# Kernel optimization log

Measured on AMD Instinct MI355X. Metric: run time of the kernel, lower is better.

Reference implementation:

```python
import jax, jax.numpy as jnp
import numpy as np

HEAD_NUM = 16
PAD = 0.0
MASKS_FUTURE = True


def setup_inputs() -> dict:
    key = jax.random.key(0)
    ks = jax.random.split(key, 7)
    B, S, D = 2, 2048, 1024
    scale = 0.02
    return {
        "q": jax.random.normal(ks[0], (B, S, D), dtype=jnp.float32),
        "k": jax.random.normal(ks[1], (B, S, D), dtype=jnp.float32),
        "v": jax.random.normal(ks[2], (B, S, D), dtype=jnp.float32),
        "w_q": jax.random.normal(ks[3], (D, D), dtype=jnp.float32) * scale,
        "w_k": jax.random.normal(ks[4], (D, D), dtype=jnp.float32) * scale,
        "w_v": jax.random.normal(ks[5], (D, D), dtype=jnp.float32) * scale,
        "w_o": jax.random.normal(ks[6], (D, D), dtype=jnp.float32) * scale,
    }


def _split_head(x):
    # [B, S, D] -> [B, H, S, D/H]
    B, S, D = x.shape
    return x.reshape(B, S, HEAD_NUM, D // HEAD_NUM).transpose(0, 2, 1, 3)


def reference(q, k, v, w_q, w_k, w_v, w_o):
    qp = _split_head(q @ w_q)  # [B, H, Sq, dk]
    kp = _split_head(k @ w_k)  # [B, H, Sk, dk]
    vp = _split_head(v @ w_v)  # [B, H, Sk, dv]
    d_k = qp.shape[-1]
    scores = jnp.einsum("bhqd,bhkd->bhqk", qp, kp) / jnp.sqrt(jnp.float32(d_k))
    # mask where scores equal PAD (faithful to tf.equal(head_qk, PAD))
    mask = scores == PAD
    if MASKS_FUTURE:
        # tf.linalg.band_part(mask, -1, 0): keep lower triangle, zero elsewhere
        Sq, Sk = scores.shape[-2], scores.shape[-1]
        tril = jnp.tril(jnp.ones((Sq, Sk), dtype=bool))
        mask = mask & tril
    neg = jnp.finfo(jnp.float32).min
    scores = jnp.where(mask, neg, scores)
    attn = jax.nn.softmax(scores, axis=-1)
    # keep_prob = 1.0 -> dropout is identity
    attn = jnp.where(mask, PAD, attn)
    out = jnp.einsum("bhqk,bhkd->bhqd", attn, vp)  # [B, H, Sq, dv/H]
    B, H, S, dh = out.shape
    concat = out.transpose(0, 2, 1, 3).reshape(B, S, H * dh)
    return concat @ w_o
```

## Files before the change

### kernel.cpp

```cpp
#include <hip/hip_runtime.h>
#include <hip/hip_bf16.h>

typedef unsigned short u16;
typedef unsigned int u32;
typedef short short8 __attribute__((ext_vector_type(8)));
typedef float float4v __attribute__((ext_vector_type(4)));
typedef u32 u32x2 __attribute__((ext_vector_type(2)));

#define SEQ 2048
#define DIM 1024
#define NHEAD 16
#define MROWS 4096
#define NE ((size_t)MROWS * DIM)
#define WN ((size_t)DIM * DIM)

#if __has_builtin(__builtin_amdgcn_exp2f)
#define EXP2(x) __builtin_amdgcn_exp2f(x)
#else
#define EXP2(x) exp2f(x)
#endif

__device__ inline u16 f2bf(float f) {
    union { float f; unsigned u; } v; v.f = f;
    unsigned r = v.u + 0x7fffu + ((v.u >> 16) & 1u);
    return (u16)(r >> 16);
}
__device__ inline float bf2f(u16 s) {
    union { unsigned u; float f; } v; v.u = ((unsigned)s) << 16;
    return v.f;
}
__device__ inline u32 pk2bf(float a, float b) {
    union { __hip_bfloat162 h; u32 u; } cv;
    cv.h = __float22bfloat162_rn(float2{a, b});
    return cv.u;
}
__device__ inline void gld16(const void* g, void* l) {
    __builtin_amdgcn_global_load_lds(
        (const __attribute__((address_space(1))) void*)g,
        (__attribute__((address_space(3))) void*)l, 16, 0, 0);
}

__global__ __launch_bounds__(256) void prep(
    const float* __restrict__ q, const float* __restrict__ k,
    const float* __restrict__ v, const float* __restrict__ w_q,
    const float* __restrict__ w_k, const float* __restrict__ w_v,
    const float* __restrict__ w_o, u16* __restrict__ Abf, u16* __restrict__ Wt)
{
    __shared__ u16 T[64 * 66];
    const int bx = blockIdx.x;
    const int tid = threadIdx.x;

    if (bx < 6144) {
        const int z = bx >> 11, xb = bx & 2047;
        const float* s = (z == 0) ? q : (z == 1) ? k : v;
        const size_t i = ((size_t)xb * 256 + tid) * 8;
        float4v a = *(const float4v*)(s + i);
        float4v b = *(const float4v*)(s + i + 4);
        short8 o;
        for (int e = 0; e < 4; e++) { o[e] = (short)f2bf(a[e]); o[4 + e] = (short)f2bf(b[e]); }
        *(short8*)(Abf + (size_t)z * NE + i) = o;
        return;
    }

    const int t = bx - 6144;
    const int z = t & 3, tile = t >> 2;
    const float* src = (z == 0) ? w_o : (z == 1) ? w_q : (z == 2) ? w_k : w_v;
    const int kt = (tile >> 4) * 64, nt = (tile & 15) * 64;
    {
        const int row = tid >> 2, cg = (tid & 3) * 16;
        const float* sp = src + (size_t)(kt + row) * DIM + nt + cg;
        for (int i4 = 0; i4 < 4; i4++) {
            float4v f = *(const float4v*)(sp + i4 * 4);
            for (int e = 0; e < 4; e++)
                T[row * 66 + cg + i4 * 4 + e] = f2bf(f[e]);
        }
    }
    __syncthreads();
    {
        const int nr = tid >> 2, kg = (tid & 3) * 16;
        u16* dp = Wt + (size_t)z * WN + (size_t)(nt + nr) * DIM + kt + kg;
        short8 o0, o1;
        for (int e = 0; e < 8; e++) {
            o0[e] = (short)T[(kg + e) * 66 + nr];
            o1[e] = (short)T[(kg + 8 + e) * 66 + nr];
        }
        *(short8*)(dp) = o0;
        *(short8*)(dp + 8) = o1;
    }
}

__global__ __launch_bounds__(256) void gemm_qkv(
    const u16* __restrict__ Abf, const u16* __restrict__ Wtg, u16* __restrict__ QKVb)
{
    __shared__ u16 SMEM[2 * 128 * 64];
    u16* Alds = SMEM;
    u16* Wlds = SMEM + 128 * 64;

    const int z = blockIdx.z;
    const u16* A = Abf + (size_t)z * NE;
    const u16* W = Wtg + (size_t)(z + 1) * WN;

    const int tid = threadIdx.x;
    const int lane = tid & 63, w = tid >> 6;
    const int quad = lane >> 4, l16 = lane & 15;
    const int wr = w >> 1, wc = w & 1;
    const int m0 = blockIdx.x * 128, n0 = blockIdx.y * 128;

    float4v acc[4][4];
    float4v vz = {0.f, 0.f, 0.f, 0.f};
    for (int i = 0; i < 4; i++)
        for (int j = 0; j < 4; j++) acc[i][j] = vz;

    for (int k0 = 0; k0 < DIM; k0 += 64) {
        for (int i = 0; i < 4; i++) {
            const int c = tid + i * 256;
            const int row = c >> 3, scc = (c & 7) ^ (row & 7);
            gld16(A + (size_t)(m0 + row) * DIM + k0 + scc * 8, &Alds[c * 8]);
            gld16(W + (size_t)(n0 + row) * DIM + k0 + scc * 8, &Wlds[c * 8]);
        }
        __syncthreads();

        for (int s = 0; s < 2; s++) {
            short8 a[4], b[4];
            for (int i = 0; i < 4; i++) {
                const int row = wr * 64 + i * 16 + l16;
                a[i] = *(const short8*)&Alds[row * 64 + (((s * 4 + quad) ^ (row & 7)) * 8)];
            }
            for (int j = 0; j < 4; j++) {
                const int row = wc * 64 + j * 16 + l16;
                b[j] = *(const short8*)&Wlds[row * 64 + (((s * 4 + quad) ^ (row & 7)) * 8)];
            }
            for (int i = 0; i < 4; i++)
                for (int j = 0; j < 4; j++)
                    acc[i][j] = __builtin_amdgcn_mfma_f32_16x16x32_bf16(a[i], b[j], acc[i][j], 0, 0, 0);
        }
        __syncthreads();
    }

    if (z < 2) {
        const float sc = (z == 0) ? 0.125f * 1.44269504088896f : 1.0f;
        for (int i = 0; i < 4; i++) {
            int row = m0 + wr * 64 + i * 16 + quad * 4;
            for (int j = 0; j < 4; j++) {
                int col = n0 + wc * 64 + j * 16 + l16;
                for (int r = 0; r < 4; r++)
                    QKVb[(size_t)z * NE + (size_t)(row + r) * DIM + col] = f2bf(acc[i][j][r] * sc);
            }
        }
        return;
    }

    u16* T = SMEM;
    for (int i = 0; i < 4; i++)
        for (int j = 0; j < 4; j++) {
            const int d = wc * 64 + j * 16 + l16;
            for (int r = 0; r < 4; r++) {
                const int s = wr * 64 + i * 16 + quad * 4 + r;
                T[d * 128 + (((s >> 3) ^ (d & 7)) * 8) + (s & 7)] = f2bf(acc[i][j][r]);
            }
        }
    __syncthreads();
    {
        u16* Vt = QKVb + 2 * NE;
        const int b = m0 >> 11, s_loc = m0 & 2047, h0 = n0 >> 6;
        const int c = lane & 15;
        for (int p = 0; p < 8; p++) {
            const int d = w * 32 + (lane >> 4) * 8 + p;
            short8 val = *(const short8*)&T[d * 128 + ((c ^ (d & 7)) * 8)];
            u16* dp = Vt + ((size_t)(b * 16 + h0 + (d >> 6)) * 64 + (d & 63)) * SEQ + s_loc + c * 8;
            *(short8*)dp = val;
        }
    }
}

__global__ __launch_bounds__(256) void gemm_out(
    const u16* __restrict__ Cb, const u16* __restrict__ Wtg, float* __restrict__ out)
{
    __shared__ u16 Alds[64 * 64];
    __shared__ u16 Wlds[128 * 64];
    const u16* W = Wtg;

    const int tid = threadIdx.x;
    const int lane = tid & 63, w = tid >> 6;
    const int quad = lane >> 4, l16 = lane & 15;
    const int wr = w >> 1, wc = w & 1;
    const int m0 = blockIdx.x * 64, n0 = blockIdx.y * 128;

    float4v acc[2][4];
    float4v vz = {0.f, 0.f, 0.f, 0.f};
    for (int i = 0; i < 2; i++)
        for (int j = 0; j < 4; j++) acc[i][j] = vz;

    for (int k0 = 0; k0 < DIM; k0 += 64) {
        for (int i = 0; i < 2; i++) {
            const int c = tid + i * 256;
            const int row = c >> 3, scc = (c & 7) ^ (row & 7);
            gld16(Cb + (size_t)(m0 + row) * DIM + k0 + scc * 8, &Alds[c * 8]);
        }
        for (int i = 0; i < 4; i++) {
            const int c = tid + i * 256;
            const int row = c >> 3, scc = (c & 7) ^ (row & 7);
            gld16(W + (size_t)(n0 + row) * DIM + k0 + scc * 8, &Wlds[c * 8]);
        }
        __syncthreads();

        for (int s = 0; s < 2; s++) {
            short8 a[2], b[4];
            for (int i = 0; i < 2; i++) {
                const int row = wr * 32 + i * 16 + l16;
                a[i] = *(const short8*)&Alds[row * 64 + (((s * 4 + quad) ^ (row & 7)) * 8)];
            }
            for (int j = 0; j < 4; j++) {
                const int row = wc * 64 + j * 16 + l16;
                b[j] = *(const short8*)&Wlds[row * 64 + (((s * 4 + quad) ^ (row & 7)) * 8)];
            }
            for (int i = 0; i < 2; i++)
                for (int j = 0; j < 4; j++)
                    acc[i][j] = __builtin_amdgcn_mfma_f32_16x16x32_bf16(a[i], b[j], acc[i][j], 0, 0, 0);
        }
        __syncthreads();
    }

    for (int i = 0; i < 2; i++) {
        int row = m0 + wr * 32 + i * 16 + quad * 4;
        for (int j = 0; j < 4; j++) {
            int col = n0 + wc * 64 + j * 16 + l16;
            for (int r = 0; r < 4; r++)
                out[(size_t)(row + r) * DIM + col] = acc[i][j][r];
        }
    }
}

__global__ __launch_bounds__(256, 4) void attn_kernel(
    const u16* __restrict__ Q, const u16* __restrict__ K,
    const u16* __restrict__ Vtg, u16* __restrict__ O)
{
    __shared__ u16 Klds[128 * 64];
    __shared__ u16 Vt[64 * 128];
    __shared__ float Llds[4][32];
    float* bufA = (float*)Klds;
    float* bufB = (float*)Vt;

    const int bh = blockIdx.x;
    const int q0 = blockIdx.y * 32;
    const int tid = threadIdx.x;
    const int lane = tid & 63, w = tid >> 6;
    const int quad = lane >> 4, l16 = lane & 15;

    const size_t base = (size_t)(bh >> 4) * SEQ * DIM + (bh & 15) * 64;
    const u16* Qp = Q + base;
    const u16* Kp = K + base;
    u16* Op = O + base;
    const u16* Vp = Vtg + (size_t)bh * 64 * SEQ;

    short8 qb[2][2];
    for (int qc = 0; qc < 2; qc++)
        for (int s = 0; s < 2; s++)
            qb[qc][s] = *(const short8*)(Qp + (size_t)(q0 + qc * 16 + l16) * DIM + s * 32 + quad * 8);

    float4v acc[2][4];
    float4v vz = {0.f, 0.f, 0.f, 0.f};
    for (int qc = 0; qc < 2; qc++)
        for (int nb = 0; nb < 4; nb++) acc[qc][nb] = vz;
    float lp[2] = {0.f, 0.f};

    u16* pw = Klds + w * 32 * 64;

    for (int kt = 0; kt < SEQ / 128; kt++) {
        const int k0 = kt * 128;
        for (int i = 0; i < 4; i++) {
            const int ck = tid + i * 256;
            const int rk = ck >> 3, sk = (ck & 7) ^ (rk & 7);
            gld16(Kp + (size_t)(k0 + rk) * DIM + sk * 8, &Klds[ck * 8]);
            const int cv = tid + i * 256;
            const int dv = cv >> 4, pv = cv & 15;
            const int sv = (pv & 8) | ((pv ^ (dv & 7)) & 7);
            gld16(Vp + (size_t)dv * SEQ + k0 + sv * 8, &Vt[cv * 8]);
        }
        __syncthreads();

        short8 ka[2][2];
        for (int kr = 0; kr < 2; kr++) {
            const int row = w * 32 + kr * 16 + l16;
            ka[kr][0] = *(const short8*)&Klds[row * 64 + ((quad ^ (l16 & 7)) * 8)];
            ka[kr][1] = *(const short8*)&Klds[row * 64 + (((4 + quad) ^ (l16 & 7)) * 8)];
        }

        float4v st[2][2];
        for (int kr = 0; kr < 2; kr++)
            for (int qc = 0; qc < 2; qc++) {
                float4v t = __builtin_amdgcn_mfma_f32_16x16x32_bf16(ka[kr][0], qb[qc][0], vz, 0, 0, 0);
                st[kr][qc] = __builtin_amdgcn_mfma_f32_16x16x32_bf16(ka[kr][1], qb[qc][1], t, 0, 0, 0);
            }

        for (int kr = 0; kr < 2; kr++)
            for (int qc = 0; qc < 2; qc++) {
                float p0 = EXP2(st[kr][qc][0]), p1 = EXP2(st[kr][qc][1]);
                float p2 = EXP2(st[kr][qc][2]), p3 = EXP2(st[kr][qc][3]);
                lp[qc] += (p0 + p1) + (p2 + p3);
                u32x2 pk; pk[0] = pk2bf(p0, p1); pk[1] = pk2bf(p2, p3);
                *(u32x2*)((u32*)pw + (qc * 16 + l16) * 20 + kr * 8 + quad * 2) = pk;
            }
        asm volatile("" ::: "memory");

        short8 pa[2], vb[4];
        for (int qc = 0; qc < 2; qc++)
            pa[qc] = *(const short8*)&pw[(qc * 16 + l16) * 40 + quad * 8];
        for (int nb = 0; nb < 4; nb++) {
            const int gk = w * 4 + quad;
            const int pos = (gk & 8) | ((gk ^ (l16 & 7)) & 7);
            vb[nb] = *(const short8*)&Vt[(nb * 16 + l16) * 128 + pos * 8];
        }
        for (int qc = 0; qc < 2; qc++)
            for (int nb = 0; nb < 4; nb++)
                acc[qc][nb] = __builtin_amdgcn_mfma_f32_16x16x32_bf16(pa[qc], vb[nb], acc[qc][nb], 0, 0, 0);
        __syncthreads();
    }

    for (int qc = 0; qc < 2; qc++) {
        lp[qc] += __shfl_xor(lp[qc], 16);
        lp[qc] += __shfl_xor(lp[qc], 32);
    }
    if (quad == 0)
        for (int qc = 0; qc < 2; qc++) Llds[w][qc * 16 + l16] = lp[qc];

    if (w == 0 || w == 2) {
        float* buf = (w == 0) ? bufA : bufB;
        for (int qc = 0; qc < 2; qc++)
            for (int nb = 0; nb < 4; nb++)
                for (int r = 0; r < 4; r++)
                    buf[(qc * 16 + quad * 4 + r) * 64 + nb * 16 + l16] = acc[qc][nb][r];
    }
    __syncthreads();
    if (w == 1 || w == 3) {
        float* buf = (w == 1) ? bufA : bufB;
        for (int qc = 0; qc < 2; qc++)
            for (int nb = 0; nb < 4; nb++)
                for (int r = 0; r < 4; r++)
                    buf[(qc * 16 + quad * 4 + r) * 64 + nb * 16 + l16] += acc[qc][nb][r];
    }
    __syncthreads();

    {
        const int q = tid >> 3, dg = (tid & 7) * 8;
        const float l = Llds[0][q] + Llds[1][q] + Llds[2][q] + Llds[3][q];
        const float inv = 1.0f / l;
        short8 o;
        for (int e = 0; e < 8; e++)
            o[e] = (short)f2bf((bufA[q * 64 + dg + e] + bufB[q * 64 + dg + e]) * inv);
        *(short8*)(Op + (size_t)(q0 + q) * DIM + dg) = o;
    }
}

extern "C" void kernel_launch(void* const* d_in, const int* in_sizes, int n_in,
                              void* d_out, int out_size, void* d_ws, size_t ws_size,
                              hipStream_t stream)
{
    const float* q   = (const float*)d_in[0];
    const float* k   = (const float*)d_in[1];
    const float* v   = (const float*)d_in[2];
    const float* w_q = (const float*)d_in[3];
    const float* w_k = (const float*)d_in[4];
    const float* w_v = (const float*)d_in[5];
    const float* w_o = (const float*)d_in[6];
    float* out = (float*)d_out;

    u16* Abf  = (u16*)d_ws;
    u16* Wt   = Abf + 3 * NE;
    u16* QKVb = Wt + 4 * WN;
    u16* Cb   = Abf;

    dim3 blk(256);
    prep<<<dim3(7168), blk, 0, stream>>>(q, k, v, w_q, w_k, w_v, w_o, Abf, Wt);
    gemm_qkv<<<dim3(32, 8, 3), blk, 0, stream>>>(Abf, Wt, QKVb);
    attn_kernel<<<dim3(32, 64), blk, 0, stream>>>(QKVb, QKVb + NE, QKVb + 2 * NE, Cb);
    gemm_out<<<dim3(64, 8), blk, 0, stream>>>(Cb, Wt, out);
}
```

Before: 233.0 us.

## Load K and V fragments directly from global memory, dropping LDS staging

Each wave now reads its K and V MFMA operands straight from global memory into registers instead of cooperatively staging 128-key K and V tiles through shared memory. This removes both per-iteration __syncthreads barriers and shrinks LDS use to a per-wave P buffer, which may allow higher occupancy. In exchange, each access is an uncoalesced 16-byte strided global load on the critical path with no prefetch. Any latency hiding now depends on the cache and on occupancy.

```diff
diff --git a/kernel.cpp b/kernel.cpp
--- a/kernel.cpp
+++ b/kernel.cpp
@@ -235,11 +235,10 @@
     const u16* __restrict__ Q, const u16* __restrict__ K,
     const u16* __restrict__ Vtg, u16* __restrict__ O)
 {
-    __shared__ u16 Klds[128 * 64];
-    __shared__ u16 Vt[64 * 128];
+    __shared__ u16 Pbuf[4][2048];
     __shared__ float Llds[4][32];
-    float* bufA = (float*)Klds;
-    float* bufB = (float*)Vt;
+    float* bufA = (float*)&Pbuf[0][0];
+    float* bufB = (float*)&Pbuf[2][0];
 
     const int bh = blockIdx.x;
     const int q0 = blockIdx.y * 32;
@@ -258,32 +257,28 @@
         for (int s = 0; s < 2; s++)
             qb[qc][s] = *(const short8*)(Qp + (size_t)(q0 + qc * 16 + l16) * DIM + s * 32 + quad * 8);
 
+    const u16* krow[2];
+    for (int kr = 0; kr < 2; kr++)
+        krow[kr] = Kp + (size_t)(w * 32 + kr * 16 + l16) * DIM + quad * 8;
+    const u16* vrow[4];
+    for (int nb = 0; nb < 4; nb++)
+        vrow[nb] = Vp + (size_t)(nb * 16 + l16) * SEQ + w * 32 + quad * 8;
+
     float4v acc[2][4];
     float4v vz = {0.f, 0.f, 0.f, 0.f};
     for (int qc = 0; qc < 2; qc++)
         for (int nb = 0; nb < 4; nb++) acc[qc][nb] = vz;
     float lp[2] = {0.f, 0.f};
 
-    u16* pw = Klds + w * 32 * 64;
+    u16* pw = Pbuf[w];
 
     for (int kt = 0; kt < SEQ / 128; kt++) {
         const int k0 = kt * 128;
-        for (int i = 0; i < 4; i++) {
-            const int ck = tid + i * 256;
-            const int rk = ck >> 3, sk = (ck & 7) ^ (rk & 7);
-            gld16(Kp + (size_t)(k0 + rk) * DIM + sk * 8, &Klds[ck * 8]);
-            const int cv = tid + i * 256;
-            const int dv = cv >> 4, pv = cv & 15;
-            const int sv = (pv & 8) | ((pv ^ (dv & 7)) & 7);
-            gld16(Vp + (size_t)dv * SEQ + k0 + sv * 8, &Vt[cv * 8]);
-        }
-        __syncthreads();
 
         short8 ka[2][2];
         for (int kr = 0; kr < 2; kr++) {
-            const int row = w * 32 + kr * 16 + l16;
-            ka[kr][0] = *(const short8*)&Klds[row * 64 + ((quad ^ (l16 & 7)) * 8)];
-            ka[kr][1] = *(const short8*)&Klds[row * 64 + (((4 + quad) ^ (l16 & 7)) * 8)];
+            ka[kr][0] = *(const short8*)(krow[kr] + (size_t)(k0) * DIM);
+            ka[kr][1] = *(const short8*)(krow[kr] + (size_t)(k0) * DIM + 32);
         }
 
         float4v st[2][2];
@@ -292,6 +287,10 @@
                 float4v t = __builtin_amdgcn_mfma_f32_16x16x32_bf16(ka[kr][0], qb[qc][0], vz, 0, 0, 0);
                 st[kr][qc] = __builtin_amdgcn_mfma_f32_16x16x32_bf16(ka[kr][1], qb[qc][1], t, 0, 0, 0);
             }
+
+        short8 vb[4];
+        for (int nb = 0; nb < 4; nb++)
+            vb[nb] = *(const short8*)(vrow[nb] + k0);
 
         for (int kr = 0; kr < 2; kr++)
             for (int qc = 0; qc < 2; qc++) {
@@ -303,18 +302,13 @@
             }
         asm volatile("" ::: "memory");
 
-        short8 pa[2], vb[4];
+        short8 pa[2];
         for (int qc = 0; qc < 2; qc++)
             pa[qc] = *(const short8*)&pw[(qc * 16 + l16) * 40 + quad * 8];
-        for (int nb = 0; nb < 4; nb++) {
-            const int gk = w * 4 + quad;
-            const int pos = (gk & 8) | ((gk ^ (l16 & 7)) & 7);
-            vb[nb] = *(const short8*)&Vt[(nb * 16 + l16) * 128 + pos * 8];
-        }
+
         for (int qc = 0; qc < 2; qc++)
             for (int nb = 0; nb < 4; nb++)
                 acc[qc][nb] = __builtin_amdgcn_mfma_f32_16x16x32_bf16(pa[qc], vb[nb], acc[qc][nb], 0, 0, 0);
-        __syncthreads();
     }
 
     for (int qc = 0; qc < 2; qc++) {
@@ -323,6 +317,7 @@
     }
     if (quad == 0)
         for (int qc = 0; qc < 2; qc++) Llds[w][qc * 16 + l16] = lp[qc];
+    __syncthreads();
 
     if (w == 0 || w == 2) {
         float* buf = (w == 0) ? bufA : bufB;
```

Measured after the change: 285.5 us. +22.5%, slower.
